# Kernel tuning notes

Hardware: AMD Instinct MI355X
Metric: run time of the kernel (lower is better)

Reference implementation:

```python
import jax, jax.numpy as jnp
import numpy as np

DIM = 768
HEADS = 12
HEAD_DIM = DIM // HEADS
EPS = 1e-5


def setup_inputs() -> dict:
    key = jax.random.key(0)
    ks = jax.random.split(key, 9)
    s = 0.02
    x = jax.random.normal(ks[0], (4, 1024, DIM), dtype=jnp.float32)
    return {
        "x": x,
        "Wqkv_c": jax.random.normal(ks[1], (DIM, 3 * DIM), jnp.float32) * s,
        "bqkv_c": jnp.zeros((3 * DIM,), jnp.float32),
        "Wp_c": jax.random.normal(ks[2], (DIM, DIM), jnp.float32) * s,
        "bp_c": jnp.zeros((DIM,), jnp.float32),
        "Wqkv_ac": jax.random.normal(ks[3], (DIM, 3 * DIM), jnp.float32) * s,
        "bqkv_ac": jnp.zeros((3 * DIM,), jnp.float32),
        "Wp_ac": jax.random.normal(ks[4], (DIM, DIM), jnp.float32) * s,
        "bp_ac": jnp.zeros((DIM,), jnp.float32),
        "gamma": jnp.ones((DIM,), jnp.float32),
        "beta": jnp.zeros((DIM,), jnp.float32),
    }


def _branch(x, Wqkv, bqkv, Wp, bp, causal: bool):
    B, T, C = x.shape
    qkv = (x @ Wqkv + bqkv).reshape(B, T, 3, HEADS, HEAD_DIM)
    qkv = jnp.transpose(qkv, (2, 0, 3, 1, 4))  # [3,B,H,T,Dh]
    q, k, v = qkv[0], qkv[1], qkv[2]
    scores = jnp.einsum("bhqd,bhkd->bhqk", q, k) / np.sqrt(HEAD_DIM).astype(np.float32)
    i = jnp.arange(T)[:, None]
    j = jnp.arange(T)[None, :]
    mask = (j <= i) if causal else (j >= i)  # tril / triu (incl. diagonal)
    scores = jnp.where(mask[None, None], scores, -jnp.inf)
    attn = jax.nn.softmax(scores, axis=-1)
    out = jnp.einsum("bhqk,bhkd->bhqd", attn, v)
    out = jnp.transpose(out, (0, 2, 1, 3)).reshape(B, T, C)
    return out @ Wp + bp


def reference(x, Wqkv_c, bqkv_c, Wp_c, bp_c, Wqkv_ac, bqkv_ac, Wp_ac, bp_ac, gamma, beta):
    out_c = _branch(x, Wqkv_c, bqkv_c, Wp_c, bp_c, causal=True)
    out_ac = _branch(x, Wqkv_ac, bqkv_ac, Wp_ac, bp_ac, causal=False)
    y = x + out_c + out_ac  # residual; dropout is identity at eval
    mu = jnp.mean(y, axis=-1, keepdims=True)
    var = jnp.var(y, axis=-1, keepdims=True)
    return (y - mu) * jax.lax.rsqrt(var + EPS) * gamma + beta
```

## Files before the change

kernel.cpp:

```cpp
#include <hip/hip_runtime.h>
#include <stdint.h>

#define DIM 768
#define HEADS 12
#define HD 64
#define BATCH 4
#define SEQ 1024
#define NTOK (BATCH*SEQ)
#define QKVW (3*DIM)
#define QKW (2*DIM)
#define EPS 1e-5f

typedef __attribute__((ext_vector_type(8))) short short8;
typedef __attribute__((ext_vector_type(4))) float f32x4;

__device__ __forceinline__ unsigned short f2bf(float f) {
    union { float f; unsigned u; } v; v.f = f;
    unsigned r = v.u + 0x7fffu + ((v.u >> 16) & 1u);
    return (unsigned short)(r >> 16);
}
__device__ __forceinline__ float b2f(unsigned short s) {
    union { unsigned u; float f; } v; v.u = (unsigned)s << 16; return v.f;
}

__device__ __forceinline__ void gld_lds16(const void* g, void* l) {
    auto gp = reinterpret_cast<const __attribute__((address_space(1))) unsigned int*>(
        (uintptr_t)g);
    auto lp = reinterpret_cast<__attribute__((address_space(3))) unsigned int*>(
        (unsigned int)(uintptr_t)l);
    __builtin_amdgcn_global_load_lds(gp, lp, 16, 0, 0);
}

#define CVT_X_BLOCKS (NTOK*DIM/4096)
#define CVT_WQ_TILES ((QKVW/32)*(DIM/32))
#define CVT_WP_TILES ((DIM/32)*(DIM/32))
__global__ __launch_bounds__(256) void cvt_all_kernel(
    const float* __restrict__ x,
    const float* __restrict__ Wq0, const float* __restrict__ Wq1,
    const float* __restrict__ Wp0, const float* __restrict__ Wp1,
    unsigned short* __restrict__ xb,
    unsigned short* __restrict__ WqT0, unsigned short* __restrict__ WqT1,
    unsigned short* __restrict__ WpT0, unsigned short* __restrict__ WpT1)
{
    const int bid = blockIdx.x, tid = threadIdx.x;
    if (bid < CVT_X_BLOCKS) {
        const int base = bid * 1024 + tid;
#pragma unroll
        for (int u = 0; u < 4; ++u) {
            const float4 v = ((const float4*)x)[base + u * 256];
            ushort4 o4;
            o4.x = f2bf(v.x); o4.y = f2bf(v.y); o4.z = f2bf(v.z); o4.w = f2bf(v.w);
            ((ushort4*)xb)[base + u * 256] = o4;
        }
        return;
    }
    __shared__ float t[32][33];
    const float* W; unsigned short* WT; int N, K, tile;
    int w = bid - CVT_X_BLOCKS;
    if (w < 2 * CVT_WQ_TILES) {
        const int z = w / CVT_WQ_TILES; tile = w % CVT_WQ_TILES;
        W = z ? Wq1 : Wq0; WT = z ? WqT1 : WqT0; N = QKVW; K = DIM;
    } else {
        w -= 2 * CVT_WQ_TILES;
        const int z = w / CVT_WP_TILES; tile = w % CVT_WP_TILES;
        W = z ? Wp1 : Wp0; WT = z ? WpT1 : WpT0; N = DIM; K = DIM;
    }
    const int ntiles = N / 32;
    const int n0 = (tile % ntiles) * 32, k0 = (tile / ntiles) * 32;
    const int c = tid & 31, rr = tid >> 5;
#pragma unroll
    for (int i = 0; i < 4; ++i)
        t[rr + 8 * i][c] = W[(size_t)(k0 + rr + 8 * i) * N + n0 + c];
    __syncthreads();
#pragma unroll
    for (int i = 0; i < 4; ++i)
        WT[(size_t)(n0 + rr + 8 * i) * K + k0 + c] = f2bf(t[c][rr + 8 * i]);
}

__global__ __launch_bounds__(256, 2) void gemm_qkv_kernel(
    const unsigned short* __restrict__ A,
    const unsigned short* __restrict__ BT0, const unsigned short* __restrict__ BT1,
    const float* __restrict__ bias0, const float* __restrict__ bias1,
    unsigned short* __restrict__ QK0, unsigned short* __restrict__ QK1,
    unsigned short* __restrict__ VT0, unsigned short* __restrict__ VT1)
{
    const int gid = blockIdx.x;
    const int g = gid & 7, l = gid >> 3;
    const int by  = (g >> 2) * 16 + (l & 15);
    const int bxz = (g & 3) * 9 + (l >> 4);
    const int z = (bxz >= 18) ? 1 : 0;
    const int bx = z ? bxz - 18 : bxz;
    const unsigned short* __restrict__ BT = z ? BT1 : BT0;
    const float* __restrict__ bias = z ? bias1 : bias0;
    unsigned short* __restrict__ QK = z ? QK1 : QK0;
    unsigned short* __restrict__ VT = z ? VT1 : VT0;
    const int m0 = by * 128;
    const int nb0 = bx * 128;

    __shared__ __align__(16) unsigned short lds[32768];

    const int tid = threadIdx.x, lane = tid & 63, wv = tid >> 6;
    const int fm = lane & 15, fg = lane >> 4;
    const int wr = wv >> 1, wc = wv & 1;

    const int sr8 = lane >> 3;
    const int sc = ((lane & 7) ^ sr8) * 8;
    const unsigned short* pA = A  + (size_t)(m0  + wv * 8 + sr8) * DIM + sc;
    const unsigned short* pB = BT + (size_t)(nb0 + wv * 8 + sr8) * DIM + sc;
    unsigned short* dA = lds + wv * 512;
    unsigned short* dB = lds + 16384 + wv * 512;

    const int swz = fm & 7;
    const int cK0 = ((0 + fg) ^ swz) * 8;
    const int cK1 = ((4 + fg) ^ swz) * 8;
    const int aB = (wr * 64 + fm) * 64;
    const int bB = (wc * 64 + fm) * 64;

    f32x4 acc[4][4];
#pragma unroll
    for (int i = 0; i < 4; ++i)
#pragma unroll
        for (int j = 0; j < 4; ++j) acc[i][j] = f32x4{0.f, 0.f, 0.f, 0.f};

    short8 a[4][2], b[4][2];

#pragma unroll
    for (int j = 0; j < 4; ++j) {
        gld_lds16(pA + j * 32 * DIM, dA + j * 2048);
        gld_lds16(pB + j * 32 * DIM, dB + j * 2048);
    }

    for (int t = 0; t < 12; ++t) {
        const int ab = (t & 1) * 8192;
        const int bb = 16384 + (t & 1) * 8192;
        const int nb2 = ((t + 1) & 1) * 8192;

        asm volatile("s_waitcnt vmcnt(0)" ::: "memory");
        __builtin_amdgcn_s_barrier();
        if (t < 11) {
            const int kN = (t + 1) * 64;
#pragma unroll
            for (int j = 0; j < 4; ++j) {
                gld_lds16(pA + kN + j * 32 * DIM, dA + nb2 + j * 2048);
                gld_lds16(pB + kN + j * 32 * DIM, dB + nb2 + j * 2048);
            }
        }

#pragma unroll
        for (int mi = 0; mi < 4; ++mi) {
            a[mi][0] = *(const short8*)&lds[ab + aB + mi * 1024 + cK0];
            a[mi][1] = *(const short8*)&lds[ab + aB + mi * 1024 + cK1];
        }
#pragma unroll
        for (int nj = 0; nj < 2; ++nj) {
            b[nj][0] = *(const short8*)&lds[bb + bB + nj * 1024 + cK0];
            b[nj][1] = *(const short8*)&lds[bb + bB + nj * 1024 + cK1];
        }
        asm volatile("s_waitcnt lgkmcnt(0)" ::: "memory");
        __builtin_amdgcn_sched_barrier(0);
        __builtin_amdgcn_s_setprio(1);
#pragma unroll
        for (int ks = 0; ks < 2; ++ks)
#pragma unroll
            for (int mi = 0; mi < 4; ++mi)
#pragma unroll
                for (int nj = 0; nj < 2; ++nj)
                    acc[mi][nj] = __builtin_amdgcn_mfma_f32_16x16x32_bf16(
                        a[mi][ks], b[nj][ks], acc[mi][nj], 0, 0, 0);
        __builtin_amdgcn_s_setprio(0);

#pragma unroll
        for (int nj = 2; nj < 4; ++nj) {
            b[nj][0] = *(const short8*)&lds[bb + bB + nj * 1024 + cK0];
            b[nj][1] = *(const short8*)&lds[bb + bB + nj * 1024 + cK1];
        }
        asm volatile("s_waitcnt lgkmcnt(0)" ::: "memory");
        __builtin_amdgcn_sched_barrier(0);
        __builtin_amdgcn_s_setprio(1);
#pragma unroll
        for (int ks = 0; ks < 2; ++ks)
#pragma unroll
            for (int mi = 0; mi < 4; ++mi)
#pragma unroll
                for (int nj = 2; nj < 4; ++nj)
                    acc[mi][nj] = __builtin_amdgcn_mfma_f32_16x16x32_bf16(
                        a[mi][ks], b[nj][ks], acc[mi][nj], 0, 0, 0);
        __builtin_amdgcn_s_setprio(0);
    }

    __syncthreads();
    const int rowg = tid >> 4, lseg = tid & 15;
    if (nb0 < QKW) {
        const float qsc = (nb0 < DIM) ? 0.125f : 1.0f;
#pragma unroll
        for (int i = 0; i < 4; ++i) {
            const int ml = wr * 64 + i * 16 + fg * 4;
#pragma unroll
            for (int j = 0; j < 4; ++j) {
                const int nl = wc * 64 + j * 16 + fm;
                const float bs = bias[nb0 + nl];
#pragma unroll
                for (int r = 0; r < 4; ++r)
                    lds[(ml + r) * 136 + nl] = f2bf((acc[i][j][r] + bs) * qsc);
            }
        }
        __syncthreads();
#pragma unroll
        for (int pp = 0; pp < 8; ++pp) {
            const int row = pp * 16 + rowg;
            const uint4 v = *(const uint4*)&lds[row * 136 + lseg * 8];
            *(uint4*)(QK + (size_t)(m0 + row) * QKW + nb0 + lseg * 8) = v;
        }
    } else {
        const int b8 = m0 >> 10, t0 = m0 & 1023;
#pragma unroll
        for (int i = 0; i < 4; ++i) {
            const int tl = wr * 64 + i * 16 + fg * 4;
#pragma unroll
            for (int j = 0; j < 4; ++j) {
                const int nl = wc * 64 + j * 16 + fm;
                const float bs = bias[nb0 + nl];
                uint2 u;
                u.x = (unsigned)f2bf(acc[i][j][0] + bs) | ((unsigned)f2bf(acc[i][j][1] + bs) << 16);
                u.y = (unsigned)f2bf(acc[i][j][2] + bs) | ((unsigned)f2bf(acc[i][j][3] + bs) << 16);
                *(uint2*)(&lds[nl * 136 + tl]) = u;
            }
        }
        __syncthreads();
#pragma unroll
        for (int pp = 0; pp < 8; ++pp) {
            const int nl = pp * 16 + rowg;
            const int nh = (nb0 - QKW) + nl;
            const uint4 v = *(const uint4*)&lds[nl * 136 + lseg * 8];
            *(uint4*)(VT + ((size_t)((b8 * HEADS + (nh >> 6)) * HD + (nh & 63))) * SEQ
                      + t0 + lseg * 8) = v;
        }
    }
}

__global__ __launch_bounds__(256) void gemm_proj_kernel(
    const unsigned short* __restrict__ A0, const unsigned short* __restrict__ BT0,
    const unsigned short* __restrict__ A1, const unsigned short* __restrict__ BT1,
    const float* __restrict__ b0, const float* __restrict__ b1,
    const float* __restrict__ xres, float* __restrict__ Y)
{
    __shared__ __align__(16) unsigned short Als[2][2][64 * 32];
    __shared__ __align__(16) unsigned short Bls[2][2][128 * 32];
    const int tid = threadIdx.x, lane = tid & 63, wv = tid >> 6;
    const int m0 = blockIdx.y * 64, n0 = blockIdx.x * 128;
    const int fm = lane & 15, fg = lane >> 4, fk = (lane >> 4) * 8;
    const int srw = lane >> 2, kk = (lane & 3) * 8;
    const int K = DIM;

    const unsigned short* Ag0  = A0  + (size_t)(m0 + wv * 16 + srw) * K + kk;
    const unsigned short* Ag1  = A1  + (size_t)(m0 + wv * 16 + srw) * K + kk;
    const unsigned short* Bg00 = BT0 + (size_t)(n0 + wv * 32 + srw) * K + kk;
    const unsigned short* Bg01 = BT0 + (size_t)(n0 + wv * 32 + 16 + srw) * K + kk;
    const unsigned short* Bg10 = BT1 + (size_t)(n0 + wv * 32 + srw) * K + kk;
    const unsigned short* Bg11 = BT1 + (size_t)(n0 + wv * 32 + 16 + srw) * K + kk;

    f32x4 acc0[4][2], acc1[4][2];
#pragma unroll
    for (int i = 0; i < 4; ++i)
#pragma unroll
        for (int j = 0; j < 2; ++j) {
            acc0[i][j] = f32x4{0.f, 0.f, 0.f, 0.f};
            acc1[i][j] = f32x4{0.f, 0.f, 0.f, 0.f};
        }

    gld_lds16(Ag0,  &Als[0][0][wv * 512]);
    gld_lds16(Bg00, &Bls[0][0][wv * 1024]);
    gld_lds16(Bg01, &Bls[0][0][wv * 1024 + 512]);
    gld_lds16(Ag1,  &Als[1][0][wv * 512]);
    gld_lds16(Bg10, &Bls[1][0][wv * 1024]);
    gld_lds16(Bg11, &Bls[1][0][wv * 1024 + 512]);

    const int NK = K / 32;
    for (int kt = 0; kt < NK; ++kt) {
        const int p = kt & 1;
        __syncthreads();
        if (kt + 1 < NK) {
            const int off = (kt + 1) * 32;
            gld_lds16(Ag0 + off,  &Als[0][p ^ 1][wv * 512]);
            gld_lds16(Bg00 + off, &Bls[0][p ^ 1][wv * 1024]);
            gld_lds16(Bg01 + off, &Bls[0][p ^ 1][wv * 1024 + 512]);
            gld_lds16(Ag1 + off,  &Als[1][p ^ 1][wv * 512]);
            gld_lds16(Bg10 + off, &Bls[1][p ^ 1][wv * 1024]);
            gld_lds16(Bg11 + off, &Bls[1][p ^ 1][wv * 1024 + 512]);
        }
        short8 af[4], bf[2];
#pragma unroll
        for (int i = 0; i < 4; ++i)
            af[i] = *(const short8*)&Als[0][p][(i * 16 + fm) * 32 + fk];
#pragma unroll
        for (int j = 0; j < 2; ++j)
            bf[j] = *(const short8*)&Bls[0][p][(wv * 32 + j * 16 + fm) * 32 + fk];
#pragma unroll
        for (int i = 0; i < 4; ++i)
#pragma unroll
            for (int j = 0; j < 2; ++j)
                acc0[i][j] = __builtin_amdgcn_mfma_f32_16x16x32_bf16(af[i], bf[j], acc0[i][j], 0, 0, 0);
#pragma unroll
        for (int i = 0; i < 4; ++i)
            af[i] = *(const short8*)&Als[1][p][(i * 16 + fm) * 32 + fk];
#pragma unroll
        for (int j = 0; j < 2; ++j)
            bf[j] = *(const short8*)&Bls[1][p][(wv * 32 + j * 16 + fm) * 32 + fk];
#pragma unroll
        for (int i = 0; i < 4; ++i)
#pragma unroll
            for (int j = 0; j < 2; ++j)
                acc1[i][j] = __builtin_amdgcn_mfma_f32_16x16x32_bf16(af[i], bf[j], acc1[i][j], 0, 0, 0);
    }
#pragma unroll
    for (int i = 0; i < 4; ++i) {
        const int m = m0 + i * 16 + fg * 4;
#pragma unroll
        for (int j = 0; j < 2; ++j) {
            const int n = n0 + wv * 32 + j * 16 + fm;
            const float bs = b0[n] + b1[n];
#pragma unroll
            for (int r = 0; r < 4; ++r) {
                const size_t idx = (size_t)(m + r) * DIM + n;
                Y[idx] = acc0[i][j][r] + acc1[i][j][r] + xres[idx] + bs;
            }
        }
    }
}

#define KP 72
__global__ __launch_bounds__(256, 3) void attn_fused_kernel(
    const unsigned short* __restrict__ qk_c, const unsigned short* __restrict__ vT_c,
    const unsigned short* __restrict__ qk_ac, const unsigned short* __restrict__ vT_ac,
    unsigned short* __restrict__ o_c, unsigned short* __restrict__ o_ac)
{
    __shared__ __align__(16) unsigned short Kls[2][64 * KP];
    __shared__ __align__(16) unsigned short Vls[2][64 * KP];
    __shared__ __align__(16) unsigned short Ps[4][16 * KP];
    const int tid = threadIdx.x, lane = tid & 63, w = tid >> 6;
    const int fm = lane & 15, fg = lane >> 4;
    const int bh = blockIdx.x, qt = blockIdx.y;
    const int b = bh / HEADS, h = bh % HEADS;
    unsigned short* Psw = &Ps[w][0];
    const int srow = tid >> 3, sseg = (tid & 7) * 8;

    for (int br = 0; br < 2; ++br) {
        const int causal = (br == 0);
        const unsigned short* __restrict__ qk = causal ? qk_c : qk_ac;
        const unsigned short* __restrict__ vT = causal ? vT_c : vT_ac;
        unsigned short* __restrict__ o = causal ? o_c : o_ac;
        const unsigned short* qbase = qk + (size_t)b * SEQ * QKW + h * HD;
        const unsigned short* kbase = qbase + DIM;
        const unsigned short* vtb   = vT + (size_t)(b * HEADS + h) * HD * SEQ;

        short8 qb0, qb1;
        {
            const size_t qoff = (size_t)(qt * 64 + w * 16 + fm) * QKW + fg * 8;
            qb0 = *(const short8*)(qbase + qoff);
            qb1 = *(const short8*)(qbase + qoff + 32);
        }

        float ls = 0.f;
        f32x4 accO[4];
#pragma unroll
        for (int dj = 0; dj < 4; ++dj) accO[dj] = f32x4{0.f, 0.f, 0.f, 0.f};

        const int ktb = causal ? 0 : qt;
        const int kte = causal ? qt : (SEQ / 64 - 1);

        uint4 kr0 = *(const uint4*)(kbase + (size_t)(ktb * 64 + srow) * QKW + sseg);
        uint4 kr1 = *(const uint4*)(kbase + (size_t)(ktb * 64 + srow + 32) * QKW + sseg);
        uint4 vr0 = *(const uint4*)(vtb + (size_t)srow * SEQ + ktb * 64 + sseg);
        uint4 vr1 = *(const uint4*)(vtb + (size_t)(srow + 32) * SEQ + ktb * 64 + sseg);

        if (br) __syncthreads();
        int p = 0;
        for (int kt = ktb; kt <= kte; ++kt) {
            *(uint4*)(&Kls[p][srow * KP + sseg])        = kr0;
            *(uint4*)(&Kls[p][(srow + 32) * KP + sseg]) = kr1;
            *(uint4*)(&Vls[p][srow * KP + sseg])        = vr0;
            *(uint4*)(&Vls[p][(srow + 32) * KP + sseg]) = vr1;
            if (kt < kte) {
                const int ktn = kt + 1;
                kr0 = *(const uint4*)(kbase + (size_t)(ktn * 64 + srow) * QKW + sseg);
                kr1 = *(const uint4*)(kbase + (size_t)(ktn * 64 + srow + 32) * QKW + sseg);
                vr0 = *(const uint4*)(vtb + (size_t)srow * SEQ + ktn * 64 + sseg);
                vr1 = *(const uint4*)(vtb + (size_t)(srow + 32) * SEQ + ktn * 64 + sseg);
            }
            __syncthreads();

            f32x4 st[4];
#pragma unroll
            for (int kj = 0; kj < 4; ++kj) {
                const short8 ka0 = *(const short8*)&Kls[p][(kj * 16 + fm) * KP + fg * 8];
                const short8 ka1 = *(const short8*)&Kls[p][(kj * 16 + fm) * KP + 32 + fg * 8];
                st[kj] = __builtin_amdgcn_mfma_f32_16x16x32_bf16(ka0, qb0, f32x4{0.f,0.f,0.f,0.f}, 0, 0, 0);
                st[kj] = __builtin_amdgcn_mfma_f32_16x16x32_bf16(ka1, qb1, st[kj], 0, 0, 0);
            }
            const bool diag = (kt == qt);
#pragma unroll
            for (int kj = 0; kj < 4; ++kj) {
                float e[4];
#pragma unroll
                for (int r = 0; r < 4; ++r) {
                    float v = st[kj][r];
                    if (diag) {
                        const int ki = kj * 16 + fg * 4 + r;
                        const int qi = w * 16 + fm;
                        const bool ok = causal ? (ki <= qi) : (ki >= qi);
                        if (!ok) v = -1e30f;
                    }
                    e[r] = __expf(v);
                    ls += e[r];
                }
                union { float f; unsigned u; } u0, u1, u2, u3;
                u0.f = e[0]; u1.f = e[1]; u2.f = e[2]; u3.f = e[3];
                uint2 u;
                u.x = (u0.u >> 16) | (u1.u & 0xffff0000u);
                u.y = (u2.u >> 16) | (u3.u & 0xffff0000u);
                *(uint2*)(Psw + fm * KP + kj * 16 + fg * 4) = u;
            }
            const short8 ap0 = *(const short8*)(Psw + fm * KP + fg * 8);
            const short8 ap1 = *(const short8*)(Psw + fm * KP + 32 + fg * 8);
#pragma unroll
            for (int dj = 0; dj < 4; ++dj) {
                const short8 vb0 = *(const short8*)&Vls[p][(dj * 16 + fm) * KP + fg * 8];
                const short8 vb1 = *(const short8*)&Vls[p][(dj * 16 + fm) * KP + 32 + fg * 8];
                accO[dj] = __builtin_amdgcn_mfma_f32_16x16x32_bf16(ap0, vb0, accO[dj], 0, 0, 0);
                accO[dj] = __builtin_amdgcn_mfma_f32_16x16x32_bf16(ap1, vb1, accO[dj], 0, 0, 0);
            }
            p ^= 1;
        }

        float lt = ls;
        lt += __shfl_xor(lt, 16);
        lt += __shfl_xor(lt, 32);
        float li_o[4];
#pragma unroll
        for (int r = 0; r < 4; ++r) li_o[r] = __shfl(lt, fg * 4 + r);
#pragma unroll
        for (int r = 0; r < 4; ++r) {
            const float inv = 1.f / li_o[r];
            const int q = qt * 64 + w * 16 + fg * 4 + r;
            unsigned short* orow = o + ((size_t)b * SEQ + q) * DIM + h * HD;
#pragma unroll
            for (int dj = 0; dj < 4; ++dj)
                orow[dj * 16 + fm] = f2bf(accO[dj][r] * inv);
        }
    }
}

__global__ __launch_bounds__(256) void ln_kernel(
    const float* __restrict__ Y,
    const float* __restrict__ gamma, const float* __restrict__ beta,
    float* __restrict__ out)
{
    const int row = blockIdx.x;
    const int tid = threadIdx.x;
    const float* yr = Y + (size_t)row * DIM;
    float v0 = yr[tid];
    float v1 = yr[tid + 256];
    float v2 = yr[tid + 512];
    float s = v0 + v1 + v2;
    float q = v0 * v0 + v1 * v1 + v2 * v2;
#pragma unroll
    for (int off = 32; off > 0; off >>= 1) {
        s += __shfl_down(s, off);
        q += __shfl_down(q, off);
    }
    __shared__ float rs_[4], rq_[4];
    const int wv = tid >> 6;
    if ((tid & 63) == 0) { rs_[wv] = s; rq_[wv] = q; }
    __syncthreads();
    const float ts = rs_[0] + rs_[1] + rs_[2] + rs_[3];
    const float tq = rq_[0] + rq_[1] + rq_[2] + rq_[3];
    const float mu = ts * (1.f / DIM);
    const float var = tq * (1.f / DIM) - mu * mu;
    const float rstd = rsqrtf(var + EPS);
    out[(size_t)row * DIM + tid]       = (v0 - mu) * rstd * gamma[tid]       + beta[tid];
    out[(size_t)row * DIM + tid + 256] = (v1 - mu) * rstd * gamma[tid + 256] + beta[tid + 256];
    out[(size_t)row * DIM + tid + 512] = (v2 - mu) * rstd * gamma[tid + 512] + beta[tid + 512];
}

extern "C" void kernel_launch(void* const* d_in, const int* in_sizes, int n_in,
                              void* d_out, int out_size, void* d_ws, size_t ws_size,
                              hipStream_t stream)
{
    const float* x       = (const float*)d_in[0];
    const float* Wqkv_c  = (const float*)d_in[1];
    const float* bqkv_c  = (const float*)d_in[2];
    const float* Wp_c    = (const float*)d_in[3];
    const float* bp_c    = (const float*)d_in[4];
    const float* Wqkv_ac = (const float*)d_in[5];
    const float* bqkv_ac = (const float*)d_in[6];
    const float* Wp_ac   = (const float*)d_in[7];
    const float* bp_ac   = (const float*)d_in[8];
    const float* gamma   = (const float*)d_in[9];
    const float* beta    = (const float*)d_in[10];
    float* out = (float*)d_out;

    char* p = (char*)d_ws;
    unsigned short* qk_c   = (unsigned short*)p; p += (size_t)NTOK * QKW * 2;
    unsigned short* qk_ac  = (unsigned short*)p; p += (size_t)NTOK * QKW * 2;
    unsigned short* vT_c   = (unsigned short*)p; p += (size_t)NTOK * DIM * 2;
    unsigned short* vT_ac  = (unsigned short*)p; p += (size_t)NTOK * DIM * 2;
    unsigned short* o_ac   = (unsigned short*)p; p += (size_t)NTOK * DIM * 2;
    unsigned short* xb     = (unsigned short*)p; p += (size_t)NTOK * DIM * 2;
    unsigned short* WqT_c  = (unsigned short*)p; p += (size_t)QKVW * DIM * 2;
    unsigned short* WqT_ac = (unsigned short*)p; p += (size_t)QKVW * DIM * 2;
    unsigned short* WpT_c  = (unsigned short*)p; p += (size_t)DIM * DIM * 2;
    unsigned short* WpT_ac = (unsigned short*)p; p += (size_t)DIM * DIM * 2;
    unsigned short* o_c = WqT_c;
    float*          Y   = (float*)qk_c;

    cvt_all_kernel<<<CVT_X_BLOCKS + 2 * CVT_WQ_TILES + 2 * CVT_WP_TILES, 256, 0, stream>>>(
        x, Wqkv_c, Wqkv_ac, Wp_c, Wp_ac, xb, WqT_c, WqT_ac, WpT_c, WpT_ac);

    gemm_qkv_kernel<<<1152, 256, 0, stream>>>(
        xb, WqT_c, WqT_ac, bqkv_c, bqkv_ac, qk_c, qk_ac, vT_c, vT_ac);

    attn_fused_kernel<<<dim3(BATCH * HEADS, SEQ / 64), 256, 0, stream>>>(
        qk_c, vT_c, qk_ac, vT_ac, o_c, o_ac);

    gemm_proj_kernel<<<dim3(DIM / 128, NTOK / 64), 256, 0, stream>>>(
        o_c, WpT_c, o_ac, WpT_ac, bp_c, bp_ac, x, Y);
    ln_kernel<<<NTOK, 256, 0, stream>>>(Y, gamma, beta, out);
}
```

Measured before the change: 188.7 us.

## Stage attention K/V tiles via direct global-to-LDS loads with XOR swizzle

Replaces the register-staged K/V tile prefetch in the fused attention kernel with direct global-to-LDS loads (gld_lds16) into unpadded 64-wide tiles. It uses an XOR column swizzle to avoid LDS bank conflicts, and waits on vmcnt plus a barrier before issuing the next tile's async load. This removes the staging registers and the ds_write traffic, and it shrinks LDS use. The price is a full vmcnt(0) wait each iteration and reliance on a helper defined elsewhere.

```diff
diff --git a/kernel.cpp b/kernel.cpp
--- a/kernel.cpp
+++ b/kernel.cpp
@@ -334,15 +334,19 @@
     const unsigned short* __restrict__ qk_ac, const unsigned short* __restrict__ vT_ac,
     unsigned short* __restrict__ o_c, unsigned short* __restrict__ o_ac)
 {
-    __shared__ __align__(16) unsigned short Kls[2][64 * KP];
-    __shared__ __align__(16) unsigned short Vls[2][64 * KP];
+    __shared__ __align__(16) unsigned short Kls[2][64 * 64];
+    __shared__ __align__(16) unsigned short Vls[2][64 * 64];
     __shared__ __align__(16) unsigned short Ps[4][16 * KP];
     const int tid = threadIdx.x, lane = tid & 63, w = tid >> 6;
     const int fm = lane & 15, fg = lane >> 4;
     const int bh = blockIdx.x, qt = blockIdx.y;
     const int b = bh / HEADS, h = bh % HEADS;
     unsigned short* Psw = &Ps[w][0];
-    const int srow = tid >> 3, sseg = (tid & 7) * 8;
+    const int wv8 = w * 8;
+    const int sr8 = lane >> 3;
+    const int scw = ((lane & 7) ^ sr8) * 8;
+    const int c0 = (fg ^ (fm & 7)) * 8;
+    const int c1 = ((4 | fg) ^ (fm & 7)) * 8;
 
     for (int br = 0; br < 2; ++br) {
         const int causal = (br == 0);
@@ -368,32 +372,30 @@
         const int ktb = causal ? 0 : qt;
         const int kte = causal ? qt : (SEQ / 64 - 1);
 
-        uint4 kr0 = *(const uint4*)(kbase + (size_t)(ktb * 64 + srow) * QKW + sseg);
-        uint4 kr1 = *(const uint4*)(kbase + (size_t)(ktb * 64 + srow + 32) * QKW + sseg);
-        uint4 vr0 = *(const uint4*)(vtb + (size_t)srow * SEQ + ktb * 64 + sseg);
-        uint4 vr1 = *(const uint4*)(vtb + (size_t)(srow + 32) * SEQ + ktb * 64 + sseg);
-
-        if (br) __syncthreads();
+        __syncthreads();
+
+#define ASTG(kt_, bf_) do {                                                        \
+        const unsigned short* kg_ = kbase + (size_t)((kt_) * 64 + wv8 + sr8) * QKW + scw; \
+        const unsigned short* vg_ = vtb + (size_t)(wv8 + sr8) * SEQ + (kt_) * 64 + scw;   \
+        gld_lds16(kg_,            &Kls[bf_][wv8 * 64]);                            \
+        gld_lds16(kg_ + 32 * QKW, &Kls[bf_][(wv8 + 32) * 64]);                     \
+        gld_lds16(vg_,            &Vls[bf_][wv8 * 64]);                            \
+        gld_lds16(vg_ + 32 * SEQ, &Vls[bf_][(wv8 + 32) * 64]);                     \
+    } while (0)
+
+        ASTG(ktb, 0);
+
         int p = 0;
         for (int kt = ktb; kt <= kte; ++kt) {
-            *(uint4*)(&Kls[p][srow * KP + sseg])        = kr0;
-            *(uint4*)(&Kls[p][(srow + 32) * KP + sseg]) = kr1;
-            *(uint4*)(&Vls[p][srow * KP + sseg])        = vr0;
-            *(uint4*)(&Vls[p][(srow + 32) * KP + sseg]) = vr1;
-            if (kt < kte) {
-                const int ktn = kt + 1;
-                kr0 = *(const uint4*)(kbase + (size_t)(ktn * 64 + srow) * QKW + sseg);
-                kr1 = *(const uint4*)(kbase + (size_t)(ktn * 64 + srow + 32) * QKW + sseg);
-                vr0 = *(const uint4*)(vtb + (size_t)srow * SEQ + ktn * 64 + sseg);
-                vr1 = *(const uint4*)(vtb + (size_t)(srow + 32) * SEQ + ktn * 64 + sseg);
-            }
-            __syncthreads();
+            asm volatile("s_waitcnt vmcnt(0)" ::: "memory");
+            __builtin_amdgcn_s_barrier();
+            if (kt < kte) ASTG(kt + 1, p ^ 1);
 
             f32x4 st[4];
 #pragma unroll
             for (int kj = 0; kj < 4; ++kj) {
-                const short8 ka0 = *(const short8*)&Kls[p][(kj * 16 + fm) * KP + fg * 8];
-                const short8 ka1 = *(const short8*)&Kls[p][(kj * 16 + fm) * KP + 32 + fg * 8];
+                const short8 ka0 = *(const short8*)&Kls[p][(kj * 16 + fm) * 64 + c0];
+                const short8 ka1 = *(const short8*)&Kls[p][(kj * 16 + fm) * 64 + c1];
                 st[kj] = __builtin_amdgcn_mfma_f32_16x16x32_bf16(ka0, qb0, f32x4{0.f,0.f,0.f,0.f}, 0, 0, 0);
                 st[kj] = __builtin_amdgcn_mfma_f32_16x16x32_bf16(ka1, qb1, st[kj], 0, 0, 0);
             }
@@ -424,13 +426,14 @@
             const short8 ap1 = *(const short8*)(Psw + fm * KP + 32 + fg * 8);
 #pragma unroll
             for (int dj = 0; dj < 4; ++dj) {
-                const short8 vb0 = *(const short8*)&Vls[p][(dj * 16 + fm) * KP + fg * 8];
-                const short8 vb1 = *(const short8*)&Vls[p][(dj * 16 + fm) * KP + 32 + fg * 8];
+                const short8 vb0 = *(const short8*)&Vls[p][(dj * 16 + fm) * 64 + c0];
+                const short8 vb1 = *(const short8*)&Vls[p][(dj * 16 + fm) * 64 + c1];
                 accO[dj] = __builtin_amdgcn_mfma_f32_16x16x32_bf16(ap0, vb0, accO[dj], 0, 0, 0);
                 accO[dj] = __builtin_amdgcn_mfma_f32_16x16x32_bf16(ap1, vb1, accO[dj], 0, 0, 0);
             }
             p ^= 1;
         }
+#undef ASTG
 
         float lt = ls;
         lt += __shfl_xor(lt, 16);
```

Result: no change. 191.2 us (+1.3%).

## Enlarge QKV GEMM tile to 256x128 with BK=32 staging

Applied to the files above, without the earlier changes.

The QKV projection GEMM now uses 256x128 output tiles instead of 128x128, halving the grid to 576 blocks. Each wave accumulates an 8x4 block of MFMA tiles, and the K loop runs 24 steps of 32 instead of 12 steps of 64, with a new LDS swizzle and smaller shared memory. The epilogue writes the two 128-row halves in turn through LDS. The aim is more arithmetic per byte loaded and less redundant A/B traffic, at the cost of more accumulator registers (128 floats per thread, which may hurt occupancy under launch_bounds(256,2)) and twice as many barriers per K element.

```diff
diff --git a/kernel.cpp b/kernel.cpp
--- a/kernel.cpp
+++ b/kernel.cpp
@@ -86,154 +86,153 @@
 {
     const int gid = blockIdx.x;
     const int g = gid & 7, l = gid >> 3;
-    const int by  = (g >> 2) * 16 + (l & 15);
-    const int bxz = (g & 3) * 9 + (l >> 4);
+    const int by  = (g >> 2) * 8 + (l & 7);
+    const int bxz = (g & 3) * 9 + (l >> 3);
     const int z = (bxz >= 18) ? 1 : 0;
     const int bx = z ? bxz - 18 : bxz;
     const unsigned short* __restrict__ BT = z ? BT1 : BT0;
     const float* __restrict__ bias = z ? bias1 : bias0;
     unsigned short* __restrict__ QK = z ? QK1 : QK0;
     unsigned short* __restrict__ VT = z ? VT1 : VT0;
-    const int m0 = by * 128;
+    const int m0 = by * 256;
     const int nb0 = bx * 128;
 
-    __shared__ __align__(16) unsigned short lds[32768];
+    __shared__ __align__(16) unsigned short lds[24576];
 
     const int tid = threadIdx.x, lane = tid & 63, wv = tid >> 6;
     const int fm = lane & 15, fg = lane >> 4;
     const int wr = wv >> 1, wc = wv & 1;
 
-    const int sr8 = lane >> 3;
-    const int sc = ((lane & 7) ^ sr8) * 8;
-    const unsigned short* pA = A  + (size_t)(m0  + wv * 8 + sr8) * DIM + sc;
-    const unsigned short* pB = BT + (size_t)(nb0 + wv * 8 + sr8) * DIM + sc;
+    const int s4 = lane >> 2;
+    const int sc = ((lane & 3) ^ ((lane >> 3) & 3)) * 8;
+    const unsigned short* pA = A  + (size_t)(m0  + wv * 16 + s4) * DIM + sc;
+    const unsigned short* pB = BT + (size_t)(nb0 + wv * 16 + s4) * DIM + sc;
     unsigned short* dA = lds + wv * 512;
     unsigned short* dB = lds + 16384 + wv * 512;
 
-    const int swz = fm & 7;
-    const int cK0 = ((0 + fg) ^ swz) * 8;
-    const int cK1 = ((4 + fg) ^ swz) * 8;
-    const int aB = (wr * 64 + fm) * 64;
-    const int bB = (wc * 64 + fm) * 64;
-
-    f32x4 acc[4][4];
-#pragma unroll
-    for (int i = 0; i < 4; ++i)
+    const int cR = (fg ^ ((fm >> 1) & 3)) * 8;
+    const int aB = (wr * 128 + fm) * 32;
+    const int bB = (wc * 64 + fm) * 32;
+
+    f32x4 acc[8][4];
+#pragma unroll
+    for (int i = 0; i < 8; ++i)
 #pragma unroll
         for (int j = 0; j < 4; ++j) acc[i][j] = f32x4{0.f, 0.f, 0.f, 0.f};
 
-    short8 a[4][2], b[4][2];
-
-#pragma unroll
-    for (int j = 0; j < 4; ++j) {
-        gld_lds16(pA + j * 32 * DIM, dA + j * 2048);
-        gld_lds16(pB + j * 32 * DIM, dB + j * 2048);
-    }
-
-    for (int t = 0; t < 12; ++t) {
+    short8 a[8], b[4];
+
+#define STAGE(kt, buf) do {                                        \
+        const int ko_ = (kt) * 32;                                 \
+        gld_lds16(pA + ko_,             dA + (buf) * 8192);        \
+        gld_lds16(pA + ko_ +  64 * DIM, dA + (buf) * 8192 + 2048); \
+        gld_lds16(pA + ko_ + 128 * DIM, dA + (buf) * 8192 + 4096); \
+        gld_lds16(pA + ko_ + 192 * DIM, dA + (buf) * 8192 + 6144); \
+        gld_lds16(pB + ko_,             dB + (buf) * 4096);        \
+        gld_lds16(pB + ko_ +  64 * DIM, dB + (buf) * 4096 + 2048); \
+    } while (0)
+
+    STAGE(0, 0);
+
+    for (int t = 0; t < 24; ++t) {
         const int ab = (t & 1) * 8192;
-        const int bb = 16384 + (t & 1) * 8192;
-        const int nb2 = ((t + 1) & 1) * 8192;
+        const int bb = 16384 + (t & 1) * 4096;
 
         asm volatile("s_waitcnt vmcnt(0)" ::: "memory");
         __builtin_amdgcn_s_barrier();
-        if (t < 11) {
-            const int kN = (t + 1) * 64;
-#pragma unroll
-            for (int j = 0; j < 4; ++j) {
-                gld_lds16(pA + kN + j * 32 * DIM, dA + nb2 + j * 2048);
-                gld_lds16(pB + kN + j * 32 * DIM, dB + nb2 + j * 2048);
-            }
-        }
-
-#pragma unroll
-        for (int mi = 0; mi < 4; ++mi) {
-            a[mi][0] = *(const short8*)&lds[ab + aB + mi * 1024 + cK0];
-            a[mi][1] = *(const short8*)&lds[ab + aB + mi * 1024 + cK1];
-        }
-#pragma unroll
-        for (int nj = 0; nj < 2; ++nj) {
-            b[nj][0] = *(const short8*)&lds[bb + bB + nj * 1024 + cK0];
-            b[nj][1] = *(const short8*)&lds[bb + bB + nj * 1024 + cK1];
-        }
+        if (t < 23) STAGE(t + 1, (t + 1) & 1);
+
+#pragma unroll
+        for (int mi = 0; mi < 8; ++mi)
+            a[mi] = *(const short8*)&lds[ab + aB + mi * 512 + cR];
+#pragma unroll
+        for (int nj = 0; nj < 2; ++nj)
+            b[nj] = *(const short8*)&lds[bb + bB + nj * 512 + cR];
         asm volatile("s_waitcnt lgkmcnt(0)" ::: "memory");
         __builtin_amdgcn_sched_barrier(0);
         __builtin_amdgcn_s_setprio(1);
 #pragma unroll
-        for (int ks = 0; ks < 2; ++ks)
-#pragma unroll
-            for (int mi = 0; mi < 4; ++mi)
-#pragma unroll
-                for (int nj = 0; nj < 2; ++nj)
-                    acc[mi][nj] = __builtin_amdgcn_mfma_f32_16x16x32_bf16(
-                        a[mi][ks], b[nj][ks], acc[mi][nj], 0, 0, 0);
+        for (int mi = 0; mi < 8; ++mi)
+#pragma unroll
+            for (int nj = 0; nj < 2; ++nj)
+                acc[mi][nj] = __builtin_amdgcn_mfma_f32_16x16x32_bf16(
+                    a[mi], b[nj], acc[mi][nj], 0, 0, 0);
         __builtin_amdgcn_s_setprio(0);
 
 #pragma unroll
-        for (int nj = 2; nj < 4; ++nj) {
-            b[nj][0] = *(const short8*)&lds[bb + bB + nj * 1024 + cK0];
-            b[nj][1] = *(const short8*)&lds[bb + bB + nj * 1024 + cK1];
-        }
+        for (int nj = 2; nj < 4; ++nj)
+            b[nj] = *(const short8*)&lds[bb + bB + nj * 512 + cR];
         asm volatile("s_waitcnt lgkmcnt(0)" ::: "memory");
         __builtin_amdgcn_sched_barrier(0);
         __builtin_amdgcn_s_setprio(1);
 #pragma unroll
-        for (int ks = 0; ks < 2; ++ks)
-#pragma unroll
-            for (int mi = 0; mi < 4; ++mi)
-#pragma unroll
-                for (int nj = 2; nj < 4; ++nj)
-                    acc[mi][nj] = __builtin_amdgcn_mfma_f32_16x16x32_bf16(
-                        a[mi][ks], b[nj][ks], acc[mi][nj], 0, 0, 0);
+        for (int mi = 0; mi < 8; ++mi)
+#pragma unroll
+            for (int nj = 2; nj < 4; ++nj)
+                acc[mi][nj] = __builtin_amdgcn_mfma_f32_16x16x32_bf16(
+                    a[mi], b[nj], acc[mi][nj], 0, 0, 0);
         __builtin_amdgcn_s_setprio(0);
     }
-
-    __syncthreads();
+#undef STAGE
+
     const int rowg = tid >> 4, lseg = tid & 15;
     if (nb0 < QKW) {
         const float qsc = (nb0 < DIM) ? 0.125f : 1.0f;
 #pragma unroll
-        for (int i = 0; i < 4; ++i) {
-            const int ml = wr * 64 + i * 16 + fg * 4;
-#pragma unroll
-            for (int j = 0; j < 4; ++j) {
-                const int nl = wc * 64 + j * 16 + fm;
-                const float bs = bias[nb0 + nl];
-#pragma unroll
-                for (int r = 0; r < 4; ++r)
-                    lds[(ml + r) * 136 + nl] = f2bf((acc[i][j][r] + bs) * qsc);
-            }
-        }
-        __syncthreads();
-#pragma unroll
-        for (int pp = 0; pp < 8; ++pp) {
-            const int row = pp * 16 + rowg;
-            const uint4 v = *(const uint4*)&lds[row * 136 + lseg * 8];
-            *(uint4*)(QK + (size_t)(m0 + row) * QKW + nb0 + lseg * 8) = v;
+        for (int h = 0; h < 2; ++h) {
+            __syncthreads();
+            if (wr == h) {
+#pragma unroll
+                for (int mi = 0; mi < 8; ++mi) {
+#pragma unroll
+                    for (int nj = 0; nj < 4; ++nj) {
+                        const int col = wc * 64 + nj * 16 + fm;
+                        const float bs = bias[nb0 + col];
+#pragma unroll
+                        for (int r = 0; r < 4; ++r) {
+                            const int rl = mi * 16 + fg * 4 + r;
+                            lds[rl * 136 + col] = f2bf((acc[mi][nj][r] + bs) * qsc);
+                        }
+                    }
+                }
+            }
+            __syncthreads();
+#pragma unroll
+            for (int pp = 0; pp < 8; ++pp) {
+                const int row = pp * 16 + rowg;
+                const uint4 v = *(const uint4*)&lds[row * 136 + lseg * 8];
+                *(uint4*)(QK + (size_t)(m0 + h * 128 + row) * QKW + nb0 + lseg * 8) = v;
+            }
         }
     } else {
         const int b8 = m0 >> 10, t0 = m0 & 1023;
 #pragma unroll
-        for (int i = 0; i < 4; ++i) {
-            const int tl = wr * 64 + i * 16 + fg * 4;
-#pragma unroll
-            for (int j = 0; j < 4; ++j) {
-                const int nl = wc * 64 + j * 16 + fm;
-                const float bs = bias[nb0 + nl];
-                uint2 u;
-                u.x = (unsigned)f2bf(acc[i][j][0] + bs) | ((unsigned)f2bf(acc[i][j][1] + bs) << 16);
-                u.y = (unsigned)f2bf(acc[i][j][2] + bs) | ((unsigned)f2bf(acc[i][j][3] + bs) << 16);
-                *(uint2*)(&lds[nl * 136 + tl]) = u;
-            }
-        }
-        __syncthreads();
-#pragma unroll
-        for (int pp = 0; pp < 8; ++pp) {
-            const int nl = pp * 16 + rowg;
-            const int nh = (nb0 - QKW) + nl;
-            const uint4 v = *(const uint4*)&lds[nl * 136 + lseg * 8];
-            *(uint4*)(VT + ((size_t)((b8 * HEADS + (nh >> 6)) * HD + (nh & 63))) * SEQ
-                      + t0 + lseg * 8) = v;
+        for (int h = 0; h < 2; ++h) {
+            __syncthreads();
+            if (wr == h) {
+#pragma unroll
+                for (int mi = 0; mi < 8; ++mi) {
+                    const int tl = mi * 16 + fg * 4;
+#pragma unroll
+                    for (int nj = 0; nj < 4; ++nj) {
+                        const int d = wc * 64 + nj * 16 + fm;
+                        const float bs = bias[nb0 + d];
+                        uint2 u;
+                        u.x = (unsigned)f2bf(acc[mi][nj][0] + bs) | ((unsigned)f2bf(acc[mi][nj][1] + bs) << 16);
+                        u.y = (unsigned)f2bf(acc[mi][nj][2] + bs) | ((unsigned)f2bf(acc[mi][nj][3] + bs) << 16);
+                        *(uint2*)(&lds[d * 136 + tl]) = u;
+                    }
+                }
+            }
+            __syncthreads();
+#pragma unroll
+            for (int pp = 0; pp < 8; ++pp) {
+                const int dl = pp * 16 + rowg;
+                const int dg = (nb0 - QKW) + dl;
+                const uint4 v = *(const uint4*)&lds[dl * 136 + lseg * 8];
+                *(uint4*)(VT + ((size_t)((b8 * HEADS + (dg >> 6)) * HD + (dg & 63))) * SEQ
+                          + t0 + h * 128 + lseg * 8) = v;
+            }
         }
     }
 }
@@ -516,7 +515,7 @@
     cvt_all_kernel<<<CVT_X_BLOCKS + 2 * CVT_WQ_TILES + 2 * CVT_WP_TILES, 256, 0, stream>>>(
         x, Wqkv_c, Wqkv_ac, Wp_c, Wp_ac, xb, WqT_c, WqT_ac, WpT_c, WpT_ac);
 
-    gemm_qkv_kernel<<<1152, 256, 0, stream>>>(
+    gemm_qkv_kernel<<<576, 256, 0, stream>>>(
         xb, WqT_c, WqT_ac, bqkv_c, bqkv_ac, qk_c, qk_ac, vT_c, vT_ac);
 
     attn_fused_kernel<<<dim3(BATCH * HEADS, SEQ / 64), 256, 0, stream>>>(
```

Measured after the change: 200.3 us. 1.06x slower.
